# Kernel optimization log

Measured on AMD Instinct MI355X. Metric: run time of the kernel, lower is better.

The kernel has to match this reference:

```python
import jax, jax.numpy as jnp
import numpy as np

H = W = M = 16          # 3D token grid
N = H * W * M           # 4096 tokens
D = 256                 # dims == out_dim == key/value dim == x1_dim
HC = 8                  # head_count
D2 = 2 * D              # concat width
C2 = 4 * D              # MixFFN hidden
OUT = D                 # out_dim
UP = OUT // 2           # PatchExpand output channels
B = 4


def _ln(x, g, b, eps=1e-5):
    m = jnp.mean(x, axis=-1, keepdims=True)
    v = jnp.mean(jnp.square(x - m), axis=-1, keepdims=True)
    return (x - m) / jnp.sqrt(v + eps) * g + b


def setup_inputs() -> dict:
    key = jax.random.key(0)
    ks = jax.random.split(key, 16)
    s = 0.02
    inp = {
        "x1": jax.random.normal(ks[0], (B, N, D), jnp.float32),
        "x2": jax.random.normal(ks[1], (B, N, D), jnp.float32),
        # x1_linear (x1_dim -> out_dim)
        "w_x1": s * jax.random.normal(ks[2], (D, OUT), jnp.float32),
        "b_x1": jnp.zeros((OUT,), jnp.float32),
        # CrossAttentionBlock.norm1 (shared for x1 and x2)
        "g_n1": jnp.ones((D,), jnp.float32),
        "be_n1": jnp.zeros((D,), jnp.float32),
        # Cross_Attention.reprojection: 1x1x1 Conv3d D -> 2D == channel matmul
        "w_rep": s * jax.random.normal(ks[3], (D, D2), jnp.float32),
        "b_rep": jnp.zeros((D2,), jnp.float32),
        # Cross_Attention.norm (LayerNorm 2D)
        "g_an": jnp.ones((D2,), jnp.float32),
        "be_an": jnp.zeros((D2,), jnp.float32),
        # CrossAttentionBlock.norm2 (LayerNorm 2D)
        "g_n2": jnp.ones((D2,), jnp.float32),
        "be_n2": jnp.zeros((D2,), jnp.float32),
        # MixFFN_skip fc1 (2D -> 4D), depthwise conv3d, norm1, fc2
        "w_fc1": s * jax.random.normal(ks[4], (D2, C2), jnp.float32),
        "b_fc1": jnp.zeros((C2,), jnp.float32),
        "w_dw": s * jax.random.normal(ks[5], (C2, 1, 3, 3, 3), jnp.float32),
        "b_dw": jnp.zeros((C2,), jnp.float32),
        "g_m1": jnp.ones((C2,), jnp.float32),
        "be_m1": jnp.zeros((C2,), jnp.float32),
        "w_fc2": s * jax.random.normal(ks[6], (C2, D2), jnp.float32),
        "b_fc2": jnp.zeros((D2,), jnp.float32),
        # concat_linear (2*dims -> out_dim)
        "w_cat": s * jax.random.normal(ks[7], (D2, OUT), jnp.float32),
        "b_cat": jnp.zeros((OUT,), jnp.float32),
        # PatchExpand: expand (out_dim -> 4*out_dim, no bias) + LayerNorm(out_dim//2)
        "w_exp": s * jax.random.normal(ks[8], (OUT, 4 * OUT), jnp.float32),
        "g_up": jnp.ones((UP,), jnp.float32),
        "be_up": jnp.zeros((UP,), jnp.float32),
    }
    return inp


def reference(x1, x2, w_x1, b_x1, g_n1, be_n1, w_rep, b_rep, g_an, be_an,
              g_n2, be_n2, w_fc1, b_fc1, w_dw, b_dw, g_m1, be_m1,
              w_fc2, b_fc2, w_cat, b_cat, w_exp, g_up, be_up):
    b = x1.shape[0]
    hk = D // HC  # head key channels (== head value channels here)

    # x1_linear
    x1e = x1 @ w_x1 + b_x1                                 # [B,N,D]

    # shared norm1 applied to both streams
    n1 = _ln(x1e, g_n1, be_n1)
    n2 = _ln(x2, g_n1, be_n1)

    # Cross_Attention (efficient attention, softmax-normalized K/Q)
    kq = jnp.transpose(n2, (0, 2, 1)).reshape(b, HC, hk, N)   # keys==queries
    val = jnp.transpose(n1, (0, 2, 1)).reshape(b, HC, hk, N)
    k = jax.nn.softmax(kq, axis=3)          # softmax over tokens
    q = jax.nn.softmax(kq, axis=2)          # softmax over head channels
    ctx = jnp.einsum('bhkn,bhvn->bhkv', k, val)        # [B,HC,hk,hv]
    att = jnp.einsum('bhkv,bhkn->bhvn', ctx, q)        # [B,HC,hv,N]
    att = att.reshape(b, D, N)                          # concat heads
    # 1x1x1 Conv3d reprojection D -> 2D, then to [B,N,2D] + LayerNorm
    rep = jnp.einsum('bdn,de->bne', att, w_rep) + b_rep
    rep = _ln(rep, g_an, be_an)                         # [B,N,2D]

    # residual concat + attention
    tx = jnp.concatenate([x1e, x2], axis=2) + rep       # [B,N,2D]

    # MixFFN_skip
    h = _ln(tx, g_n2, be_n2) @ w_fc1 + b_fc1            # [B,N,C2]
    hv = jnp.transpose(h, (0, 2, 1)).reshape(b, C2, H, W, M)
    dw = jax.lax.conv_general_dilated(
        hv, w_dw, window_strides=(1, 1, 1), padding='SAME',
        feature_group_count=C2,
        dimension_numbers=('NCDHW', 'OIDHW', 'NCDHW'))
    dw = dw + b_dw[None, :, None, None, None]
    dw = jnp.transpose(dw.reshape(b, C2, N), (0, 2, 1))  # [B,N,C2]
    ax = jax.nn.gelu(_ln(dw + h, g_m1, be_m1), approximate=False)
    mx = tx + (ax @ w_fc2 + b_fc2)                       # [B,N,2D]

    # concat_linear
    y = mx @ w_cat + b_cat                               # [B,N,OUT]

    ye = y @ w_exp                                       # [B,N,4*OUT]
    ye = ye.reshape(b, 8 * N, UP)                        # view+reshape of contiguous
    out = _ln(ye, g_up, be_up)                           # [B,8N,OUT//2]
    return out
```

## Files before the change

kernel.cpp:

```cpp
#include <hip/hip_runtime.h>
#include <math.h>

using u16 = unsigned short;
typedef __bf16 bf16x8 __attribute__((ext_vector_type(8)));
typedef float f32x4 __attribute__((ext_vector_type(4)));

#define BB 4
#define NN 4096
#define DD 256
#define DD2 512
#define CC2 1024
static constexpr int ROWS = BB * NN;
static constexpr size_t MB = 1024 * 1024;

__device__ __forceinline__ u16 f2bf(float f) {
  union { float f; unsigned u; } v; v.f = f;
  unsigned r = v.u + 0x7fffu + ((v.u >> 16) & 1u);
  return (u16)(r >> 16);
}
__device__ __forceinline__ float bf2f(u16 u) {
  union { unsigned u; float f; } v; v.u = ((unsigned)u) << 16;
  return v.f;
}
__device__ __forceinline__ float u2f(unsigned x) {
  union { unsigned u; float f; } v; v.u = x; return v.f;
}
__device__ __forceinline__ void gload16(const void* g, void* l) {
  __builtin_amdgcn_global_load_lds(
      (const __attribute__((address_space(1))) void*)g,
      (__attribute__((address_space(3))) void*)l, 16, 0, 0);
}

__global__ __launch_bounds__(256) void wprep_all(
    const float* __restrict__ w_x1, const float* __restrict__ w_rep,
    const float* __restrict__ w_fc1, const float* __restrict__ w_fc2,
    const float* __restrict__ w_cat, const float* __restrict__ w_exp,
    const float* __restrict__ w_dw, const float* __restrict__ b_cat,
    u16* __restrict__ w_x1t, u16* __restrict__ w_rept,
    u16* __restrict__ w_fc1t, u16* __restrict__ w_fc2t,
    u16* __restrict__ w_cat_b, u16* __restrict__ w_expt,
    float* __restrict__ w_dwt, float* __restrict__ b_comb) {
  int i = blockIdx.x * 256 + threadIdx.x;
  if (i < 65536) { int n = i >> 8, k = i & 255; w_x1t[i] = f2bf(w_x1[k * 256 + n]); return; }
  i -= 65536;
  if (i < 131072) { int n = i >> 8, k = i & 255; w_rept[i] = f2bf(w_rep[k * 512 + n]); return; }
  i -= 131072;
  if (i < 524288) { int n = i >> 9, k = i & 511; w_fc1t[i] = f2bf(w_fc1[k * 1024 + n]); return; }
  i -= 524288;
  if (i < 524288) { int n = i >> 10, k = i & 1023; w_fc2t[i] = f2bf(w_fc2[k * 512 + n]); return; }
  i -= 524288;
  if (i < 131072) { w_cat_b[i] = f2bf(w_cat[i]); return; }
  i -= 131072;
  if (i < 262144) { int n = i >> 8, k = i & 255; w_expt[i] = f2bf(w_exp[k * 1024 + n]); return; }
  i -= 262144;
  if (i < 27648) { int widx = i >> 10, c = i & 1023; w_dwt[i] = w_dw[c * 27 + widx]; return; }
  i -= 27648;
  if (i < 1024) {
    float acc = 0.f;
    for (int o = 0; o < 256; ++o) acc += b_cat[o] * w_exp[o * 1024 + i];
    b_comb[i] = acc;
  }
}

template <int K, int EPI, bool AF32 = false, bool PERB = false>
__global__ __launch_bounds__(256, 2) void gemm_mfma(
    const u16* __restrict__ A, const u16* __restrict__ Bt,
    const float* __restrict__ bias, const u16* __restrict__ resid,
    void* __restrict__ Cout, int nTilesN,
    const float* __restrict__ gup, const float* __restrict__ beup) {
  const int t = threadIdx.x;
  int bid = blockIdx.x;
  const int nwg = gridDim.x;
  if ((nwg & 7) == 0) bid = (bid & 7) * (nwg >> 3) + (bid >> 3);
  const int m0 = (bid / nTilesN) * 128;
  const int n0 = (bid % nTilesN) * 128;
  const int Ncols = nTilesN * 128;
  if (PERB) Bt += (size_t)(m0 >> 12) * (size_t)Ncols * K;
  const int lane = t & 63, wid = t >> 6;
  const int wr = wid >> 1, wc = wid & 1;
  const int lrow = lane & 15, kgrp = lane >> 4;

  __shared__ u16 ldsA[2][128 * 32];
  __shared__ u16 ldsB[2][128 * 32];

  int srow[2], sslot[2];
#pragma unroll
  for (int c = 0; c < 2; ++c) {
    int idx = c * 256 + t;
    srow[c] = idx >> 2;
    sslot[c] = (idx & 3) ^ ((srow[c] >> 1) & 3);
  }

  int offA[4], offB[4];
#pragma unroll
  for (int m = 0; m < 4; ++m) {
    int r = wr * 64 + m * 16 + lrow;
    offA[m] = r * 32 + ((kgrp ^ ((r >> 1) & 3)) * 8);
  }
#pragma unroll
  for (int n = 0; n < 4; ++n) {
    int r = wc * 64 + n * 16 + lrow;
    offB[n] = r * 32 + ((kgrp ^ ((r >> 1) & 3)) * 8);
  }

  f32x4 acc[4][4];
#pragma unroll
  for (int m = 0; m < 4; ++m)
#pragma unroll
    for (int n = 0; n < 4; ++n) acc[m][n] = f32x4{0.f, 0.f, 0.f, 0.f};

  auto loadA32 = [&](int c, int kc) -> uint4 {
    const float* A32 = (const float*)A;
    const float* p = A32 + (size_t)(m0 + srow[c]) * K + kc + sslot[c] * 8;
    float4 f0 = *(const float4*)p;
    float4 f1 = *(const float4*)(p + 4);
    u16 o[8] = {f2bf(f0.x), f2bf(f0.y), f2bf(f0.z), f2bf(f0.w),
                f2bf(f1.x), f2bf(f1.y), f2bf(f1.z), f2bf(f1.w)};
    return *(uint4*)o;
  };
  auto stage_async = [&](int buf, int kc) {
#pragma unroll
    for (int c = 0; c < 2; ++c) {
      gload16(A + (size_t)(m0 + srow[c]) * K + kc + sslot[c] * 8,
              &ldsA[buf][(c * 256 + t) * 8]);
      gload16(Bt + (size_t)(n0 + srow[c]) * K + kc + sslot[c] * 8,
              &ldsB[buf][(c * 256 + t) * 8]);
    }
  };

  uint4 ra[2], rb[2];
  if constexpr (AF32) {
#pragma unroll
    for (int c = 0; c < 2; ++c) {
      ra[c] = loadA32(c, 0);
      rb[c] = *(const uint4*)(Bt + (size_t)(n0 + srow[c]) * K + sslot[c] * 8);
    }
#pragma unroll
    for (int c = 0; c < 2; ++c) {
      int idx = c * 256 + t;
      *(uint4*)&ldsA[0][idx * 8] = ra[c];
      *(uint4*)&ldsB[0][idx * 8] = rb[c];
    }
  } else {
    stage_async(0, 0);
  }
  __syncthreads();

  const int nt = K / 32;
  for (int tt = 0; tt < nt; ++tt) {
    const int cur = tt & 1;
    if (tt + 1 < nt) {
      const int kc = (tt + 1) * 32;
      if constexpr (AF32) {
#pragma unroll
        for (int c = 0; c < 2; ++c) {
          ra[c] = loadA32(c, kc);
          rb[c] = *(const uint4*)(Bt + (size_t)(n0 + srow[c]) * K + kc + sslot[c] * 8);
        }
      } else {
        stage_async(cur ^ 1, kc);
      }
    }
    bf16x8 af[4], bf[4];
#pragma unroll
    for (int m = 0; m < 4; ++m) af[m] = *(const bf16x8*)&ldsA[cur][offA[m]];
#pragma unroll
    for (int n = 0; n < 4; ++n) bf[n] = *(const bf16x8*)&ldsB[cur][offB[n]];
#pragma unroll
    for (int m = 0; m < 4; ++m)
#pragma unroll
      for (int n = 0; n < 4; ++n)
        acc[m][n] = __builtin_amdgcn_mfma_f32_16x16x32_bf16(af[m], bf[n], acc[m][n], 0, 0, 0);
    if (AF32 && tt + 1 < nt) {
#pragma unroll
      for (int c = 0; c < 2; ++c) {
        int idx = c * 256 + t;
        *(uint4*)&ldsA[cur ^ 1][idx * 8] = ra[c];
        *(uint4*)&ldsB[cur ^ 1][idx * 8] = rb[c];
      }
    }
    __syncthreads();
  }

  if (EPI == 3) {
    float bcol3[4];
#pragma unroll
    for (int n = 0; n < 4; ++n) {
      int gc = n0 + wc * 64 + n * 16 + lrow;
      bcol3[n] = bias ? bias[gc] : 0.f;
    }
    __shared__ float lnS[2][128], lnQ[2][128];
    float s_[4][4], q_[4][4];
#pragma unroll
    for (int m = 0; m < 4; ++m)
#pragma unroll
      for (int j = 0; j < 4; ++j) {
        float s = 0.f, q = 0.f;
#pragma unroll
        for (int n = 0; n < 4; ++n) {
          float v = acc[m][n][j] + bcol3[n];
          s += v; q += v * v;
        }
        s_[m][j] = s; q_[m][j] = q;
      }
#pragma unroll
    for (int msk = 1; msk < 16; msk <<= 1) {
#pragma unroll
      for (int m = 0; m < 4; ++m)
#pragma unroll
        for (int j = 0; j < 4; ++j) {
          s_[m][j] += __shfl_xor(s_[m][j], msk, 64);
          q_[m][j] += __shfl_xor(q_[m][j], msk, 64);
        }
    }
    if (lrow == 0) {
#pragma unroll
      for (int m = 0; m < 4; ++m)
#pragma unroll
        for (int j = 0; j < 4; ++j) {
          int r = wr * 64 + m * 16 + kgrp * 4 + j;
          lnS[wc][r] = s_[m][j];
          lnQ[wc][r] = q_[m][j];
        }
    }
    __syncthreads();
#pragma unroll
    for (int m = 0; m < 4; ++m) {
      const int rb0 = wr * 64 + m * 16 + kgrp * 4;
#pragma unroll
      for (int j = 0; j < 4; ++j) {
        const int r = rb0 + j;
        float S = lnS[0][r] + lnS[1][r];
        float Q = lnQ[0][r] + lnQ[1][r];
        float mean = S * (1.0f / 128.0f);
        float var = Q * (1.0f / 128.0f) - mean * mean;
        float iv = rsqrtf(var + 1e-5f);
#pragma unroll
        for (int n = 0; n < 4; ++n) {
          int lc = wc * 64 + n * 16 + lrow;
          ((float*)Cout)[(size_t)(m0 + r) * Ncols + n0 + lc] =
              (acc[m][n][j] + bcol3[n] - mean) * iv * gup[lc] + beup[lc];
        }
      }
    }
    return;
  }

  float bcol[4];
#pragma unroll
  for (int n = 0; n < 4; ++n) {
    int col = n0 + wc * 64 + n * 16 + (lane & 15);
    bcol[n] = bias ? bias[col] : 0.f;
  }
#pragma unroll
  for (int m = 0; m < 4; ++m) {
    const int r0 = m0 + wr * 64 + m * 16 + kgrp * 4;
#pragma unroll
    for (int n = 0; n < 4; ++n) {
      const int col = n0 + wc * 64 + n * 16 + (lane & 15);
#pragma unroll
      for (int j = 0; j < 4; ++j) {
        float v = acc[m][n][j] + bcol[n];
        size_t idx = (size_t)(r0 + j) * Ncols + col;
        if (EPI == 0) {
          ((float*)Cout)[idx] = v;
        } else if (EPI == 1) {
          ((u16*)Cout)[idx] = f2bf(v);
        } else {
          v += bf2f(resid[idx]);
          ((u16*)Cout)[idx] = f2bf(v);
        }
      }
    }
  }
}

__global__ __launch_bounds__(256) void ln256_both(
    const u16* __restrict__ x1e_b, const float* __restrict__ x2,
    const float* __restrict__ g, const float* __restrict__ be,
    u16* __restrict__ n1T, u16* __restrict__ n2T, u16* __restrict__ qmat) {
  int row = blockIdx.x;
  const int t = threadIdx.x;
  const bool first = row < ROWS;
  if (!first) row -= ROWS;
  __shared__ float ws[8];
  float v = first ? bf2f(x1e_b[(size_t)row * DD + t])
                  : x2[(size_t)row * DD + t];
  float s = v, q = v * v;
#pragma unroll
  for (int m = 1; m < 64; m <<= 1) {
    s += __shfl_xor(s, m, 64);
    q += __shfl_xor(q, m, 64);
  }
  if ((t & 63) == 0) { ws[t >> 6] = s; ws[4 + (t >> 6)] = q; }
  __syncthreads();
  s = ws[0] + ws[1] + ws[2] + ws[3];
  q = ws[4] + ws[5] + ws[6] + ws[7];
  float mean = s * (1.0f / DD);
  float var = q * (1.0f / DD) - mean * mean;
  float iv = rsqrtf(var + 1e-5f);
  u16 rb = f2bf((v - mean) * iv * g[t] + be[t]);
  int b = row >> 12, n = row & 4095;
  if (first) {
    n1T[((size_t)(b * 256 + t)) * 4096 + n] = rb;
  } else {
    n2T[((size_t)(b * 256 + t)) * 4096 + n] = rb;
    float vq = bf2f(rb);
    float hm = vq;
#pragma unroll
    for (int m = 1; m < 32; m <<= 1) hm = fmaxf(hm, __shfl_xor(hm, m, 32));
    float he = __expf(vq - hm);
    float hs = he;
#pragma unroll
    for (int m = 1; m < 32; m <<= 1) hs += __shfl_xor(hs, m, 32);
    qmat[(size_t)row * DD + t] = f2bf(he / hs);
  }
}

__global__ __launch_bounds__(256) void k34_ctx(
    const u16* __restrict__ n2T, const u16* __restrict__ n1T,
    float* __restrict__ ctx) {
  const int bid = blockIdx.x;
  const int bx = (bid & 7) * 128 + (bid >> 3);
  const int b = bx >> 8, d = bx & 255;
  const int h = d >> 5, kk = d & 31;
  const int t = threadIdx.x;
  __shared__ u16 prow[4096];
  __shared__ float xred[8];
  __shared__ float sw[128];
  const u16* src = n2T + (size_t)bx * 4096;
  ((uint4*)prow)[t] = ((const uint4*)src)[t];
  ((uint4*)prow)[256 + t] = ((const uint4*)src)[256 + t];
  __syncthreads();
  float mx = -1e30f;
#pragma unroll
  for (int i = 0; i < 16; ++i) mx = fmaxf(mx, bf2f(prow[i * 256 + t]));
#pragma unroll
  for (int m = 1; m < 64; m <<= 1) mx = fmaxf(mx, __shfl_xor(mx, m, 64));
  if ((t & 63) == 0) xred[t >> 6] = mx;
  __syncthreads();
  mx = fmaxf(fmaxf(xred[0], xred[1]), fmaxf(xred[2], xred[3]));
  float sme = 0.f;
#pragma unroll
  for (int i = 0; i < 16; ++i) sme += __expf(bf2f(prow[i * 256 + t]) - mx);
#pragma unroll
  for (int m = 1; m < 64; m <<= 1) sme += __shfl_xor(sme, m, 64);
  if ((t & 63) == 0) xred[4 + (t >> 6)] = sme;
  __syncthreads();
  const float inv = 1.0f / (xred[4] + xred[5] + xred[6] + xred[7]);

  float acc[32];
#pragma unroll
  for (int v = 0; v < 32; ++v) acc[v] = 0.f;
  const u16* vbase = n1T + ((size_t)(b * 256 + h * 32)) * 4096;
  for (int i = 0; i < 16; ++i) {
    const int n = i * 256 + t;
    const float p = __expf(bf2f(prow[n]) - mx) * inv;
#pragma unroll
    for (int v = 0; v < 32; ++v)
      acc[v] += p * bf2f(vbase[(size_t)v * 4096 + n]);
  }
#pragma unroll
  for (int v = 0; v < 32; ++v) {
#pragma unroll
    for (int m = 1; m < 64; m <<= 1) acc[v] += __shfl_xor(acc[v], m, 64);
  }
  if ((t & 63) == 0) {
#pragma unroll
    for (int v = 0; v < 32; ++v) sw[(t >> 6) * 32 + v] = acc[v];
  }
  __syncthreads();
  if (t < 32)
    ctx[(((size_t)(b * 8 + h)) * 32 + kk) * 32 + t] =
        sw[t] + sw[32 + t] + sw[64 + t] + sw[96 + t];
}

__global__ __launch_bounds__(256) void m2_build(
    const float* __restrict__ ctx, const u16* __restrict__ w_rept,
    u16* __restrict__ m2t) {
  const int b = blockIdx.x >> 4, ec = blockIdx.x & 15;
  const int t = threadIdx.x;
  const int e = ec * 32 + (t >> 3), h = t & 7;
  __shared__ float cl[8192];
#pragma unroll
  for (int i = 0; i < 8; ++i)
    *(float4*)(cl + t * 32 + i * 4) = *(const float4*)(ctx + b * 8192 + t * 32 + i * 4);
  __syncthreads();
  float wf[32];
  {
    u16 wv[32];
#pragma unroll
    for (int i = 0; i < 4; ++i)
      *(uint4*)(wv + i * 8) = *(const uint4*)(w_rept + (size_t)e * 256 + h * 32 + i * 8);
#pragma unroll
    for (int v = 0; v < 32; ++v) wf[v] = bf2f(wv[v]);
  }
  u16 outv[32];
#pragma unroll
  for (int kk = 0; kk < 32; ++kk) {
    float acc = 0.f;
    const float* cp = cl + h * 1024 + kk * 32;
#pragma unroll
    for (int v = 0; v < 32; ++v) acc += cp[v] * wf[v];
    outv[kk] = f2bf(acc);
  }
  u16* dst = m2t + ((size_t)(b * 512 + e)) * 256 + h * 32;
#pragma unroll
  for (int i = 0; i < 4; ++i) *(uint4*)(dst + i * 8) = *(uint4*)(outv + i * 8);
}

__global__ __launch_bounds__(256) void l3_reptx(
    const u16* __restrict__ rep_b, const u16* __restrict__ x1e,
    const float* __restrict__ x2,
    const float* __restrict__ g_an, const float* __restrict__ be_an,
    const float* __restrict__ g_n2, const float* __restrict__ be_n2,
    u16* __restrict__ tx, u16* __restrict__ txln) {
  const int row = blockIdx.x, t = threadIdx.x;
  __shared__ float ws[8];
  float a0 = bf2f(rep_b[(size_t)row * DD2 + t]);
  float a1 = bf2f(rep_b[(size_t)row * DD2 + 256 + t]);
  float s = a0 + a1, q = a0 * a0 + a1 * a1;
#pragma unroll
  for (int m = 1; m < 64; m <<= 1) {
    s += __shfl_xor(s, m, 64);
    q += __shfl_xor(q, m, 64);
  }
  if ((t & 63) == 0) { ws[t >> 6] = s; ws[4 + (t >> 6)] = q; }
  __syncthreads();
  s = ws[0] + ws[1] + ws[2] + ws[3];
  q = ws[4] + ws[5] + ws[6] + ws[7];
  float mean = s * (1.0f / DD2);
  float var = q * (1.0f / DD2) - mean * mean;
  float iv = rsqrtf(var + 1e-5f);
  float r0 = (a0 - mean) * iv * g_an[t] + be_an[t];
  float r1 = (a1 - mean) * iv * g_an[256 + t] + be_an[256 + t];
  float t0 = bf2f(x1e[(size_t)row * DD + t]) + r0;
  float t1 = x2[(size_t)row * DD + t] + r1;
  tx[(size_t)row * DD2 + t] = f2bf(t0);
  tx[(size_t)row * DD2 + 256 + t] = f2bf(t1);
  __syncthreads();
  s = t0 + t1; q = t0 * t0 + t1 * t1;
#pragma unroll
  for (int m = 1; m < 64; m <<= 1) {
    s += __shfl_xor(s, m, 64);
    q += __shfl_xor(q, m, 64);
  }
  if ((t & 63) == 0) { ws[t >> 6] = s; ws[4 + (t >> 6)] = q; }
  __syncthreads();
  s = ws[0] + ws[1] + ws[2] + ws[3];
  q = ws[4] + ws[5] + ws[6] + ws[7];
  mean = s * (1.0f / DD2);
  var = q * (1.0f / DD2) - mean * mean;
  iv = rsqrtf(var + 1e-5f);
  txln[(size_t)row * DD2 + t] = f2bf((t0 - mean) * iv * g_n2[t] + be_n2[t]);
  txln[(size_t)row * DD2 + 256 + t] = f2bf((t1 - mean) * iv * g_n2[256 + t] + be_n2[256 + t]);
}

__global__ __launch_bounds__(1024) void c8a_col(
    const u16* __restrict__ h, const float* __restrict__ w_dwt,
    const float* __restrict__ b_dw, const float* __restrict__ g,
    const float* __restrict__ be, u16* __restrict__ ax) {
  const int bid = blockIdx.x;
  const int cidx = (bid & 7) * 128 + (bid >> 3);
  const int b = cidx >> 8, y = (cidx >> 4) & 15, x = cidx & 15;
  const int t = threadIdx.x;
  const int lane = t & 63, wave = t >> 6;
  const size_t hb = (size_t)b * NN * CC2;

  __shared__ float2 red[16][16];
  __shared__ float2 stats[16];

  int coln[9];
  float cmask[9];
#pragma unroll
  for (int dy = -1; dy <= 1; ++dy)
#pragma unroll
    for (int dx = -1; dx <= 1; ++dx) {
      int qq = (dy + 1) * 3 + (dx + 1);
      int yy = y + dy, xx = x + dx;
      bool ok = ((unsigned)yy < 16u) && ((unsigned)xx < 16u);
      coln[qq] = ((ok ? yy : y) << 4) | (ok ? xx : x);
      cmask[qq] = ok ? 1.f : 0.f;
    }

  float wr[3][9];
#pragma unroll
  for (int p = 0; p < 3; ++p)
#pragma unroll
    for (int qq = 0; qq < 9; ++qq)
      wr[p][qq] = w_dwt[(p * 9 + qq) * CC2 + t] * cmask[qq];
  const float bias = b_dw[t];

  u16 win[3][9];
#define LOADPLANE(ZL, SLOT)                                                   \
  do {                                                                        \
    if ((ZL) >= 0 && (ZL) < 16) {                                             \
      _Pragma("unroll") for (int qq = 0; qq < 9; ++qq) win[SLOT][qq] =        \
          h[hb + (size_t)((((ZL) << 8) | coln[qq])) * CC2 + t];               \
    } else {                                                                  \
      _Pragma("unroll") for (int qq = 0; qq < 9; ++qq) win[SLOT][qq] = 0;     \
    }                                                                         \
  } while (0)

  LOADPLANE(-1, 0);
  LOADPLANE(0, 1);
  LOADPLANE(1, 2);

  float vs[16];
#pragma unroll
  for (int z = 0; z < 16; ++z) {
    const int pm1 = z % 3, pz = (z + 1) % 3, pp1 = (z + 2) % 3;
    float a0 = bias;
#pragma unroll
    for (int qq = 0; qq < 9; ++qq) {
      a0 += bf2f(win[pm1][qq]) * wr[0][qq];
      a0 += bf2f(win[pz][qq]) * wr[1][qq];
      a0 += bf2f(win[pp1][qq]) * wr[2][qq];
    }
    float v = a0 + bf2f(win[pz][4]);
    LOADPLANE(z + 2, pm1);
    vs[z] = v;
    float s = v, q2 = v * v;
#pragma unroll
    for (int m = 1; m < 64; m <<= 1) {
      s += __shfl_xor(s, m, 64);
      q2 += __shfl_xor(q2, m, 64);
    }
    if (lane == 0) red[z][wave] = make_float2(s, q2);
  }
#undef LOADPLANE
  __syncthreads();

  {
    const int z = wave;
    float S = (lane < 16) ? red[z][lane].x : 0.f;
    float Q = (lane < 16) ? red[z][lane].y : 0.f;
#pragma unroll
    for (int m = 1; m < 16; m <<= 1) {
      S += __shfl_xor(S, m, 64);
      Q += __shfl_xor(Q, m, 64);
    }
    if (lane == 0) {
      float mean = S * (1.0f / CC2);
      float var = Q * (1.0f / CC2) - mean * mean;
      stats[z] = make_float2(mean, rsqrtf(var + 1e-5f));
    }
  }
  __syncthreads();

  const float gg = g[t], bb = be[t];
#pragma unroll
  for (int z = 0; z < 16; ++z) {
    float2 st = stats[z];
    float u = (vs[z] - st.x) * st.y * gg + bb;
    float s2 = 1.5957691216f * (u + 0.044715f * u * u * u);
    float o = u / (1.0f + __expf(-s2));
    ax[((size_t)(b * NN + ((z << 8) | (y << 4) | x))) * CC2 + t] = f2bf(o);
  }
}

extern "C" void kernel_launch(void* const* d_in, const int* in_sizes, int n_in,
                              void* d_out, int out_size, void* d_ws, size_t ws_size,
                              hipStream_t stream) {
  const float* x1    = (const float*)d_in[0];
  const float* x2    = (const float*)d_in[1];
  const float* w_x1  = (const float*)d_in[2];
  const float* b_x1  = (const float*)d_in[3];
  const float* g_n1  = (const float*)d_in[4];
  const float* be_n1 = (const float*)d_in[5];
  const float* w_rep = (const float*)d_in[6];
  const float* b_rep = (const float*)d_in[7];
  const float* g_an  = (const float*)d_in[8];
  const float* be_an = (const float*)d_in[9];
  const float* g_n2  = (const float*)d_in[10];
  const float* be_n2 = (const float*)d_in[11];
  const float* w_fc1 = (const float*)d_in[12];
  const float* b_fc1 = (const float*)d_in[13];
  const float* w_dw  = (const float*)d_in[14];
  const float* b_dw  = (const float*)d_in[15];
  const float* g_m1  = (const float*)d_in[16];
  const float* be_m1 = (const float*)d_in[17];
  const float* w_fc2 = (const float*)d_in[18];
  const float* b_fc2 = (const float*)d_in[19];
  const float* w_cat = (const float*)d_in[20];
  const float* b_cat = (const float*)d_in[21];
  const float* w_exp = (const float*)d_in[22];
  const float* g_up  = (const float*)d_in[23];
  const float* be_up = (const float*)d_in[24];

  char* ws = (char*)d_ws;
  float* out = (float*)d_out;

  u16*   qmat    = (u16*)(ws + 0);
  u16*   x1e_b   = (u16*)(ws + 8 * MB);
  u16*   n1T     = (u16*)(ws + 24 * MB);
  u16*   n2T     = (u16*)(ws + 40 * MB);
  float* ctx     = (float*)(ws + 48 * MB);
  u16*   rep_b   = (u16*)(ws + 49 * MB);
  u16*   tx      = (u16*)(ws + 81 * MB);
  u16*   txln    = (u16*)(ws + 97 * MB);
  u16*   hbuf    = (u16*)(ws + 113 * MB);
  u16*   ax      = (u16*)(ws + 49 * MB);
  u16*   mx      = (u16*)(ws + 8 * MB);
  u16*   w_x1t   = (u16*)(ws + 145 * MB);
  u16*   w_rept  = w_x1t + 256 * 256;
  u16*   w_fc1t  = w_rept + 512 * 256;
  u16*   w_fc2t  = w_fc1t + 1024 * 512;
  u16*   w_cat_b = w_fc2t + 512 * 1024;
  u16*   w_expt  = w_cat_b + 512 * 256;
  float* w_dwt   = (float*)(ws + 149 * MB);
  u16*   w_combT = (u16*)(ws + 150 * MB);
  float* b_comb  = (float*)(ws + 151 * MB);
  u16*   m2t     = (u16*)(ws + 152 * MB);

  wprep_all<<<(1667072 + 255) / 256, 256, 0, stream>>>(
      w_x1, w_rep, w_fc1, w_fc2, w_cat, w_exp, w_dw, b_cat,
      w_x1t, w_rept, w_fc1t, w_fc2t, w_cat_b, w_expt, w_dwt, b_comb);

  gemm_mfma<256, 1><<<32, 256, 0, stream>>>(
      w_expt, w_cat_b, nullptr, nullptr, w_combT, 4, nullptr, nullptr);

  gemm_mfma<256, 1, true><<<(ROWS / 128) * 2, 256, 0, stream>>>(
      (const u16*)x1, w_x1t, b_x1, nullptr, x1e_b, 2, nullptr, nullptr);
  ln256_both<<<2 * ROWS, 256, 0, stream>>>(x1e_b, x2, g_n1, be_n1, n1T, n2T, qmat);
  k34_ctx<<<BB * 256, 256, 0, stream>>>(n2T, n1T, ctx);
  m2_build<<<64, 256, 0, stream>>>(ctx, w_rept, m2t);
  gemm_mfma<256, 1, false, true><<<(ROWS / 128) * 4, 256, 0, stream>>>(
      qmat, m2t, b_rep, nullptr, rep_b, 4, nullptr, nullptr);
  l3_reptx<<<ROWS, 256, 0, stream>>>(rep_b, x1e_b, x2, g_an, be_an, g_n2, be_n2, tx, txln);
  gemm_mfma<512, 1><<<(ROWS / 128) * 8, 256, 0, stream>>>(
      txln, w_fc1t, b_fc1, nullptr, hbuf, 8, nullptr, nullptr);
  c8a_col<<<1024, 1024, 0, stream>>>(hbuf, w_dwt, b_dw, g_m1, be_m1, ax);
  gemm_mfma<1024, 2><<<(ROWS / 128) * 4, 256, 0, stream>>>(
      ax, w_fc2t, b_fc2, tx, mx, 4, nullptr, nullptr);
  gemm_mfma<512, 3><<<(ROWS / 128) * 8, 256, 0, stream>>>(
      mx, w_combT, b_comb, nullptr, out, 8, g_up, be_up);
}
```

Measured before the change: 327.9 us.

## Use packed fp16 for depthwise conv, split concat/expand GEMMs, drop block swizzle

The fc1 output is now stored as fp16, and the depthwise 3D conv runs in packed half2 arithmetic with two channels per thread, using 512-thread blocks. The GELU output stays fp16, so the fc2 GEMM uses f16 MFMA. The folded w_cat·w_exp weight and its bias are dropped: concat_linear now runs as its own K=512 GEMM into an intermediate buffer, followed by a K=256 expand GEMM with a LayerNorm epilogue. The GEMM workgroup swizzle is also removed. Together these trade fp16 accumulation precision in the conv, plus an extra intermediate write and read, for cheaper conv arithmetic and fewer FLOPs in the final GEMM.

```diff
diff --git a/kernel.cpp b/kernel.cpp
--- a/kernel.cpp
+++ b/kernel.cpp
@@ -3,6 +3,8 @@
 
 using u16 = unsigned short;
 typedef __bf16 bf16x8 __attribute__((ext_vector_type(8)));
+typedef _Float16 h16x8 __attribute__((ext_vector_type(8)));
+typedef _Float16 h2 __attribute__((ext_vector_type(2)));
 typedef float f32x4 __attribute__((ext_vector_type(4)));
 
 #define BB 4
@@ -22,8 +24,8 @@
   union { unsigned u; float f; } v; v.u = ((unsigned)u) << 16;
   return v.f;
 }
-__device__ __forceinline__ float u2f(unsigned x) {
-  union { unsigned u; float f; } v; v.u = x; return v.f;
+__device__ __forceinline__ u16 f2h(float f) {
+  union { _Float16 h; u16 u; } v; v.h = (_Float16)f; return v.u;
 }
 __device__ __forceinline__ void gload16(const void* g, void* l) {
   __builtin_amdgcn_global_load_lds(
@@ -35,11 +37,11 @@
     const float* __restrict__ w_x1, const float* __restrict__ w_rep,
     const float* __restrict__ w_fc1, const float* __restrict__ w_fc2,
     const float* __restrict__ w_cat, const float* __restrict__ w_exp,
-    const float* __restrict__ w_dw, const float* __restrict__ b_cat,
+    const float* __restrict__ w_dw,
     u16* __restrict__ w_x1t, u16* __restrict__ w_rept,
-    u16* __restrict__ w_fc1t, u16* __restrict__ w_fc2t,
-    u16* __restrict__ w_cat_b, u16* __restrict__ w_expt,
-    float* __restrict__ w_dwt, float* __restrict__ b_comb) {
+    u16* __restrict__ w_fc1t, u16* __restrict__ w_fc2h,
+    u16* __restrict__ w_catt, u16* __restrict__ w_expt,
+    unsigned* __restrict__ w_dwh) {
   int i = blockIdx.x * 256 + threadIdx.x;
   if (i < 65536) { int n = i >> 8, k = i & 255; w_x1t[i] = f2bf(w_x1[k * 256 + n]); return; }
   i -= 65536;
@@ -47,31 +49,28 @@
   i -= 131072;
   if (i < 524288) { int n = i >> 9, k = i & 511; w_fc1t[i] = f2bf(w_fc1[k * 1024 + n]); return; }
   i -= 524288;
-  if (i < 524288) { int n = i >> 10, k = i & 1023; w_fc2t[i] = f2bf(w_fc2[k * 512 + n]); return; }
+  if (i < 524288) { int n = i >> 10, k = i & 1023; w_fc2h[i] = f2h(w_fc2[k * 512 + n]); return; }
   i -= 524288;
-  if (i < 131072) { w_cat_b[i] = f2bf(w_cat[i]); return; }
+  if (i < 131072) { int n = i >> 9, k = i & 511; w_catt[i] = f2bf(w_cat[k * 256 + n]); return; }
   i -= 131072;
   if (i < 262144) { int n = i >> 8, k = i & 255; w_expt[i] = f2bf(w_exp[k * 1024 + n]); return; }
   i -= 262144;
-  if (i < 27648) { int widx = i >> 10, c = i & 1023; w_dwt[i] = w_dw[c * 27 + widx]; return; }
-  i -= 27648;
-  if (i < 1024) {
-    float acc = 0.f;
-    for (int o = 0; o < 256; ++o) acc += b_cat[o] * w_exp[o * 1024 + i];
-    b_comb[i] = acc;
-  }
-}
-
-template <int K, int EPI, bool AF32 = false, bool PERB = false>
+  if (i < 13824) {
+    int tap = i >> 9, cp = i & 511;
+    unsigned lo = f2h(w_dw[(2 * cp) * 27 + tap]);
+    unsigned hi = f2h(w_dw[(2 * cp + 1) * 27 + tap]);
+    w_dwh[i] = lo | (hi << 16);
+  }
+}
+
+template <int K, int EPI, bool AF32 = false, bool PERB = false, bool F16 = false>
 __global__ __launch_bounds__(256, 2) void gemm_mfma(
     const u16* __restrict__ A, const u16* __restrict__ Bt,
     const float* __restrict__ bias, const u16* __restrict__ resid,
     void* __restrict__ Cout, int nTilesN,
     const float* __restrict__ gup, const float* __restrict__ beup) {
   const int t = threadIdx.x;
-  int bid = blockIdx.x;
-  const int nwg = gridDim.x;
-  if ((nwg & 7) == 0) bid = (bid & 7) * (nwg >> 3) + (bid >> 3);
+  const int bid = blockIdx.x;
   const int m0 = (bid / nTilesN) * 128;
   const int n0 = (bid % nTilesN) * 128;
   const int Ncols = nTilesN * 128;
@@ -161,16 +160,29 @@
         stage_async(cur ^ 1, kc);
       }
     }
-    bf16x8 af[4], bf[4];
-#pragma unroll
-    for (int m = 0; m < 4; ++m) af[m] = *(const bf16x8*)&ldsA[cur][offA[m]];
-#pragma unroll
-    for (int n = 0; n < 4; ++n) bf[n] = *(const bf16x8*)&ldsB[cur][offB[n]];
-#pragma unroll
-    for (int m = 0; m < 4; ++m)
-#pragma unroll
-      for (int n = 0; n < 4; ++n)
-        acc[m][n] = __builtin_amdgcn_mfma_f32_16x16x32_bf16(af[m], bf[n], acc[m][n], 0, 0, 0);
+    if constexpr (F16) {
+      h16x8 af[4], bf[4];
+#pragma unroll
+      for (int m = 0; m < 4; ++m) af[m] = *(const h16x8*)&ldsA[cur][offA[m]];
+#pragma unroll
+      for (int n = 0; n < 4; ++n) bf[n] = *(const h16x8*)&ldsB[cur][offB[n]];
+#pragma unroll
+      for (int m = 0; m < 4; ++m)
+#pragma unroll
+        for (int n = 0; n < 4; ++n)
+          acc[m][n] = __builtin_amdgcn_mfma_f32_16x16x32_f16(af[m], bf[n], acc[m][n], 0, 0, 0);
+    } else {
+      bf16x8 af[4], bf[4];
+#pragma unroll
+      for (int m = 0; m < 4; ++m) af[m] = *(const bf16x8*)&ldsA[cur][offA[m]];
+#pragma unroll
+      for (int n = 0; n < 4; ++n) bf[n] = *(const bf16x8*)&ldsB[cur][offB[n]];
+#pragma unroll
+      for (int m = 0; m < 4; ++m)
+#pragma unroll
+        for (int n = 0; n < 4; ++n)
+          acc[m][n] = __builtin_amdgcn_mfma_f32_16x16x32_bf16(af[m], bf[n], acc[m][n], 0, 0, 0);
+    }
     if (AF32 && tt + 1 < nt) {
 #pragma unroll
       for (int c = 0; c < 2; ++c) {
@@ -183,12 +195,6 @@
   }
 
   if (EPI == 3) {
-    float bcol3[4];
-#pragma unroll
-    for (int n = 0; n < 4; ++n) {
-      int gc = n0 + wc * 64 + n * 16 + lrow;
-      bcol3[n] = bias ? bias[gc] : 0.f;
-    }
     __shared__ float lnS[2][128], lnQ[2][128];
     float s_[4][4], q_[4][4];
 #pragma unroll
@@ -198,7 +204,7 @@
         float s = 0.f, q = 0.f;
 #pragma unroll
         for (int n = 0; n < 4; ++n) {
-          float v = acc[m][n][j] + bcol3[n];
+          float v = acc[m][n][j];
           s += v; q += v * v;
         }
         s_[m][j] = s; q_[m][j] = q;
@@ -239,7 +245,7 @@
         for (int n = 0; n < 4; ++n) {
           int lc = wc * 64 + n * 16 + lrow;
           ((float*)Cout)[(size_t)(m0 + r) * Ncols + n0 + lc] =
-              (acc[m][n][j] + bcol3[n] - mean) * iv * gup[lc] + beup[lc];
+              (acc[m][n][j] - mean) * iv * gup[lc] + beup[lc];
         }
       }
     }
@@ -266,6 +272,8 @@
           ((float*)Cout)[idx] = v;
         } else if (EPI == 1) {
           ((u16*)Cout)[idx] = f2bf(v);
+        } else if (EPI == 4) {
+          ((u16*)Cout)[idx] = f2h(v);
         } else {
           v += bf2f(resid[idx]);
           ((u16*)Cout)[idx] = f2bf(v);
@@ -456,18 +464,19 @@
   txln[(size_t)row * DD2 + 256 + t] = f2bf((t1 - mean) * iv * g_n2[256 + t] + be_n2[256 + t]);
 }
 
-__global__ __launch_bounds__(1024) void c8a_col(
-    const u16* __restrict__ h, const float* __restrict__ w_dwt,
+__global__ __launch_bounds__(512) void c8a_col(
+    const u16* __restrict__ h, const unsigned* __restrict__ w_dwh,
     const float* __restrict__ b_dw, const float* __restrict__ g,
     const float* __restrict__ be, u16* __restrict__ ax) {
   const int bid = blockIdx.x;
   const int cidx = (bid & 7) * 128 + (bid >> 3);
   const int b = cidx >> 8, y = (cidx >> 4) & 15, x = cidx & 15;
   const int t = threadIdx.x;
+  const int c0 = t * 2;
   const int lane = t & 63, wave = t >> 6;
   const size_t hb = (size_t)b * NN * CC2;
 
-  __shared__ float2 red[16][16];
+  __shared__ float2 red[16][8];
   __shared__ float2 stats[16];
 
   int coln[9];
@@ -483,22 +492,26 @@
       cmask[qq] = ok ? 1.f : 0.f;
     }
 
-  float wr[3][9];
+  h2 wr[3][9];
 #pragma unroll
   for (int p = 0; p < 3; ++p)
 #pragma unroll
-    for (int qq = 0; qq < 9; ++qq)
-      wr[p][qq] = w_dwt[(p * 9 + qq) * CC2 + t] * cmask[qq];
-  const float bias = b_dw[t];
-
-  u16 win[3][9];
+    for (int qq = 0; qq < 9; ++qq) {
+      union { unsigned u; h2 h; } w;
+      w.u = w_dwh[(p * 9 + qq) * 512 + t];
+      _Float16 m = (_Float16)cmask[qq];
+      wr[p][qq] = w.h * (h2){m, m};
+    }
+  h2 bias2 = {(_Float16)b_dw[c0], (_Float16)b_dw[c0 + 1]};
+
+  union { unsigned u; h2 h; } win[3][9];
 #define LOADPLANE(ZL, SLOT)                                                   \
   do {                                                                        \
     if ((ZL) >= 0 && (ZL) < 16) {                                             \
-      _Pragma("unroll") for (int qq = 0; qq < 9; ++qq) win[SLOT][qq] =        \
-          h[hb + (size_t)((((ZL) << 8) | coln[qq])) * CC2 + t];               \
+      _Pragma("unroll") for (int qq = 0; qq < 9; ++qq) win[SLOT][qq].u =      \
+          *(const unsigned*)(h + hb + (size_t)((((ZL) << 8) | coln[qq])) * CC2 + c0); \
     } else {                                                                  \
-      _Pragma("unroll") for (int qq = 0; qq < 9; ++qq) win[SLOT][qq] = 0;     \
+      _Pragma("unroll") for (int qq = 0; qq < 9; ++qq) win[SLOT][qq].u = 0u;  \
     }                                                                         \
   } while (0)
 
@@ -506,21 +519,23 @@
   LOADPLANE(0, 1);
   LOADPLANE(1, 2);
 
-  float vs[16];
+  unsigned vs[16];
 #pragma unroll
   for (int z = 0; z < 16; ++z) {
     const int pm1 = z % 3, pz = (z + 1) % 3, pp1 = (z + 2) % 3;
-    float a0 = bias;
+    h2 acc = bias2;
 #pragma unroll
     for (int qq = 0; qq < 9; ++qq) {
-      a0 += bf2f(win[pm1][qq]) * wr[0][qq];
-      a0 += bf2f(win[pz][qq]) * wr[1][qq];
-      a0 += bf2f(win[pp1][qq]) * wr[2][qq];
-    }
-    float v = a0 + bf2f(win[pz][4]);
+      acc = win[pm1][qq].h * wr[0][qq] + acc;
+      acc = win[pz][qq].h * wr[1][qq] + acc;
+      acc = win[pp1][qq].h * wr[2][qq] + acc;
+    }
+    acc = acc + win[pz][4].h;
     LOADPLANE(z + 2, pm1);
-    vs[z] = v;
-    float s = v, q2 = v * v;
+    union { h2 h; unsigned u; } pk; pk.h = acc;
+    vs[z] = pk.u;
+    float v0 = (float)acc[0], v1 = (float)acc[1];
+    float s = v0 + v1, q2 = v0 * v0 + v1 * v1;
 #pragma unroll
     for (int m = 1; m < 64; m <<= 1) {
       s += __shfl_xor(s, m, 64);
@@ -531,31 +546,35 @@
 #undef LOADPLANE
   __syncthreads();
 
-  {
-    const int z = wave;
-    float S = (lane < 16) ? red[z][lane].x : 0.f;
-    float Q = (lane < 16) ? red[z][lane].y : 0.f;
-#pragma unroll
-    for (int m = 1; m < 16; m <<= 1) {
+  for (int zz = wave; zz < 16; zz += 8) {
+    float S = (lane < 8) ? red[zz][lane].x : 0.f;
+    float Q = (lane < 8) ? red[zz][lane].y : 0.f;
+#pragma unroll
+    for (int m = 1; m < 8; m <<= 1) {
       S += __shfl_xor(S, m, 64);
       Q += __shfl_xor(Q, m, 64);
     }
     if (lane == 0) {
       float mean = S * (1.0f / CC2);
       float var = Q * (1.0f / CC2) - mean * mean;
-      stats[z] = make_float2(mean, rsqrtf(var + 1e-5f));
-    }
-  }
-  __syncthreads();
-
-  const float gg = g[t], bb = be[t];
+      stats[zz] = make_float2(mean, rsqrtf(var + 1e-5f));
+    }
+  }
+  __syncthreads();
+
+  const float g0 = g[c0], g1 = g[c0 + 1], b0 = be[c0], b1 = be[c0 + 1];
 #pragma unroll
   for (int z = 0; z < 16; ++z) {
     float2 st = stats[z];
-    float u = (vs[z] - st.x) * st.y * gg + bb;
-    float s2 = 1.5957691216f * (u + 0.044715f * u * u * u);
-    float o = u / (1.0f + __expf(-s2));
-    ax[((size_t)(b * NN + ((z << 8) | (y << 4) | x))) * CC2 + t] = f2bf(o);
+    union { unsigned u; h2 h; } pv; pv.u = vs[z];
+    float u0 = ((float)pv.h[0] - st.x) * st.y * g0 + b0;
+    float u1 = ((float)pv.h[1] - st.x) * st.y * g1 + b1;
+    float s0 = 1.5957691216f * (u0 + 0.044715f * u0 * u0 * u0);
+    float s1 = 1.5957691216f * (u1 + 0.044715f * u1 * u1 * u1);
+    float o0 = u0 / (1.0f + __expf(-s0));
+    float o1 = u1 / (1.0f + __expf(-s1));
+    unsigned pk = (unsigned)f2h(o0) | ((unsigned)f2h(o1) << 16);
+    *(unsigned*)(ax + ((size_t)(b * NN + ((z << 8) | (y << 4) | x))) * CC2 + c0) = pk;
   }
 }
 
@@ -602,23 +621,19 @@
   u16*   hbuf    = (u16*)(ws + 113 * MB);
   u16*   ax      = (u16*)(ws + 49 * MB);
   u16*   mx      = (u16*)(ws + 8 * MB);
+  u16*   ybuf    = (u16*)(ws + 0);
   u16*   w_x1t   = (u16*)(ws + 145 * MB);
   u16*   w_rept  = w_x1t + 256 * 256;
   u16*   w_fc1t  = w_rept + 512 * 256;
-  u16*   w_fc2t  = w_fc1t + 1024 * 512;
-  u16*   w_cat_b = w_fc2t + 512 * 1024;
-  u16*   w_expt  = w_cat_b + 512 * 256;
-  float* w_dwt   = (float*)(ws + 149 * MB);
-  u16*   w_combT = (u16*)(ws + 150 * MB);
-  float* b_comb  = (float*)(ws + 151 * MB);
+  u16*   w_fc2h  = w_fc1t + 1024 * 512;
+  u16*   w_catt  = w_fc2h + 512 * 1024;
+  u16*   w_expt  = w_catt + 256 * 512;
+  unsigned* w_dwh = (unsigned*)(ws + 149 * MB);
   u16*   m2t     = (u16*)(ws + 152 * MB);
 
-  wprep_all<<<(1667072 + 255) / 256, 256, 0, stream>>>(
-      w_x1, w_rep, w_fc1, w_fc2, w_cat, w_exp, w_dw, b_cat,
-      w_x1t, w_rept, w_fc1t, w_fc2t, w_cat_b, w_expt, w_dwt, b_comb);
-
-  gemm_mfma<256, 1><<<32, 256, 0, stream>>>(
-      w_expt, w_cat_b, nullptr, nullptr, w_combT, 4, nullptr, nullptr);
+  wprep_all<<<(1652224 + 255) / 256, 256, 0, stream>>>(
+      w_x1, w_rep, w_fc1, w_fc2, w_cat, w_exp, w_dw,
+      w_x1t, w_rept, w_fc1t, w_fc2h, w_catt, w_expt, w_dwh);
 
   gemm_mfma<256, 1, true><<<(ROWS / 128) * 2, 256, 0, stream>>>(
       (const u16*)x1, w_x1t, b_x1, nullptr, x1e_b, 2, nullptr, nullptr);
@@ -628,11 +643,13 @@
   gemm_mfma<256, 1, false, true><<<(ROWS / 128) * 4, 256, 0, stream>>>(
       qmat, m2t, b_rep, nullptr, rep_b, 4, nullptr, nullptr);
   l3_reptx<<<ROWS, 256, 0, stream>>>(rep_b, x1e_b, x2, g_an, be_an, g_n2, be_n2, tx, txln);
-  gemm_mfma<512, 1><<<(ROWS / 128) * 8, 256, 0, stream>>>(
+  gemm_mfma<512, 4><<<(ROWS / 128) * 8, 256, 0, stream>>>(
       txln, w_fc1t, b_fc1, nullptr, hbuf, 8, nullptr, nullptr);
-  c8a_col<<<1024, 1024, 0, stream>>>(hbuf, w_dwt, b_dw, g_m1, be_m1, ax);
-  gemm_mfma<1024, 2><<<(ROWS / 128) * 4, 256, 0, stream>>>(
-      ax, w_fc2t, b_fc2, tx, mx, 4, nullptr, nullptr);
-  gemm_mfma<512, 3><<<(ROWS / 128) * 8, 256, 0, stream>>>(
-      mx, w_combT, b_comb, nullptr, out, 8, g_up, be_up);
-}
+  c8a_col<<<1024, 512, 0, stream>>>(hbuf, w_dwh, b_dw, g_m1, be_m1, ax);
+  gemm_mfma<1024, 2, false, false, true><<<(ROWS / 128) * 4, 256, 0, stream>>>(
+      ax, w_fc2h, b_fc2, tx, mx, 4, nullptr, nullptr);
+  gemm_mfma<512, 1><<<(ROWS / 128) * 2, 256, 0, stream>>>(
+      mx, w_catt, b_cat, nullptr, ybuf, 2, nullptr, nullptr);
+  gemm_mfma<256, 3><<<(ROWS / 128) * 8, 256, 0, stream>>>(
+      ybuf, w_expt, nullptr, nullptr, out, 8, g_up, be_up);
+}
```

New measurement: 300.7 us. 8.3% less time.
